# Kernel optimization log

Measured on AMD Instinct MI355X. Metric: run time of the kernel, lower is better.

Reference implementation:

```python
import jax, jax.numpy as jnp
import numpy as np

WINDOW = (2, 6, 12)  # (Wz, Wh, Ww), N = 144
HEADS = 6
TYPE_OF_WINDOWS = 10


def _position_index(ws):
    Wz, Wh, Ww = ws
    zi = np.arange(Wz); zj = -np.arange(Wz) * Wz
    hi = np.arange(Wh); hj = -np.arange(Wh) * Wh
    w = np.arange(Ww)
    c1 = np.stack(np.meshgrid(zi, hi, w, indexing='ij')).reshape(3, -1)
    c2 = np.stack(np.meshgrid(zj, hj, w, indexing='ij')).reshape(3, -1)
    coords = (c1[:, :, None] - c2[:, None, :]).transpose(1, 2, 0).copy()
    coords[:, :, 2] += Ww - 1
    coords[:, :, 1] *= 2 * Ww - 1
    coords[:, :, 0] *= (2 * Ww - 1) * Wh * Wh
    return coords.sum(-1).reshape(-1)  # [N*N]


def setup_inputs() -> dict:
    key = jax.random.key(0)
    ks = jax.random.split(key, 7)
    B, nW, C = 96, TYPE_OF_WINDOWS, 192
    N = WINDOW[0] * WINDOW[1] * WINDOW[2]
    bias_len = (2 * WINDOW[2] - 1) * WINDOW[1] ** 2 * WINDOW[0] ** 2
    return {
        'x': jax.random.normal(ks[0], (B, nW, N, C), jnp.float32),
        'mask': jax.random.normal(ks[1], (B, N, N), jnp.float32),
        'w_qkv': jax.random.normal(ks[2], (C, 3 * C), jnp.float32) * 0.02,
        'b_qkv': jnp.zeros((3 * C,), jnp.float32),
        'w_proj': jax.random.normal(ks[3], (C, C), jnp.float32) * 0.02,
        'b_proj': jnp.zeros((C,), jnp.float32),
        'bias_table': jax.random.normal(ks[4], (bias_len, nW, HEADS), jnp.float32) * 0.02,
        'position_index': jnp.asarray(_position_index(WINDOW), jnp.int32),
    }


def reference(x, mask, w_qkv, b_qkv, w_proj, b_proj, bias_table, position_index):
    B, nW, N, C = x.shape
    H = HEADS
    Dh = C // H
    scale = Dh ** -0.5
    qkv = x @ w_qkv + b_qkv                       # [B,nW,N,3C]
    qkv = qkv.reshape(B, nW, N, 3, H, Dh)
    qkv = qkv.transpose(3, 0, 1, 4, 2, 5)         # [3,B,nW,H,N,Dh]
    q, k, v = qkv[0], qkv[1], qkv[2]
    attn = jnp.einsum('bwhnd,bwhmd->bwhnm', q * scale, k)   # [B,nW,H,N,N]
    bias = bias_table[position_index]             # [N*N,nW,H]
    bias = bias.reshape(N, N, nW, H).transpose(2, 3, 0, 1)  # [nW,H,N,N]
    attn = attn + bias[None] + mask[:, None, None, :, :]
    attn = jax.nn.softmax(attn, axis=-1)
    out = jnp.einsum('bwhnm,bwhmd->bwhnd', attn, v)         # [B,nW,H,N,Dh]
    out = out.transpose(0, 1, 3, 2, 4).reshape(B, nW, N, C)
    return out @ w_proj + b_proj
```

## Files before the change

kernel.cpp:

```cpp
#include <hip/hip_runtime.h>
#include <hip/hip_bf16.h>
#include <math.h>

#define B_   96
#define NW   10
#define NN   144
#define CC   192
#define HH   6
#define DH   32
#define SCALE 0.17677669529663687f

#define XP 200
#define PP 152
#define NBW (B_ * NW)
#define QKV_STRIDE (NN * DH)

typedef __attribute__((ext_vector_type(8))) short v8s;
typedef __attribute__((ext_vector_type(4))) unsigned short v4us;
typedef __attribute__((ext_vector_type(4))) float v4f;

__device__ __forceinline__ unsigned short f2b(float f) {
  __hip_bfloat16 h = __float2bfloat16(f);
  return *reinterpret_cast<unsigned short*>(&h);
}
__device__ __forceinline__ float b2f(unsigned short s) {
  union { unsigned u; float f; } v; v.u = ((unsigned)s) << 16;
  return v.f;
}

#define N_WQT (576*192)
#define N_WPT (192*192)
#define N_BIAS (NW*HH*NN*NN)

__global__ __launch_bounds__(256) void prep_kernel(
    const float* __restrict__ w_qkv, const float* __restrict__ w_proj,
    const float* __restrict__ bias_table, const int* __restrict__ pos,
    unsigned short* __restrict__ wqT, unsigned short* __restrict__ wpT,
    unsigned short* __restrict__ biasNN)
{
  int i = blockIdx.x * 256 + threadIdx.x;
  if (i < N_WQT) {
    int n = i / 192, k = i % 192;
    wqT[i] = f2b(w_qkv[k * 576 + n]);
  } else if (i < N_WQT + N_WPT) {
    int j = i - N_WQT;
    int n = j / 192, k = j % 192;
    wpT[j] = f2b(w_proj[k * 192 + n]);
  } else if (i < N_WQT + N_WPT + N_BIAS) {
    int j = i - (N_WQT + N_WPT);
    int m = j % NN, n = (j / NN) % NN, h = (j / (NN * NN)) % HH, w = j / (NN * NN * HH);
    biasNN[j] = f2b(bias_table[(pos[n * NN + m] * NW + w) * HH + h]);
  }
}

__global__ __launch_bounds__(256, 2) void qkv_gemm(
    const float* __restrict__ x, const float* __restrict__ b_qkv,
    const unsigned short* __restrict__ wqT,
    unsigned short* __restrict__ qkv, int bw0)
{
  __shared__ unsigned short xs[NN * XP];
  const int tid  = threadIdx.x;
  const int wave = tid >> 6, lane = tid & 63;
  const int lr = lane & 15, lk8 = (lane >> 4) * 8, quad = lane >> 4;
  const int bwl = blockIdx.x;
  const int bw  = bw0 + bwl;

  const float4* xp4 = (const float4*)(x + (size_t)bw * NN * CC);
  for (int i = tid; i < NN * (CC / 4); i += 256) {
    float4 f = xp4[i];
    int r = i / (CC / 4), c = (i % (CC / 4)) * 4;
    v4us pk;
    pk[0] = f2b(f.x); pk[1] = f2b(f.y); pk[2] = f2b(f.z); pk[3] = f2b(f.w);
    *(v4us*)&xs[r * XP + c] = pk;
  }
  __syncthreads();

  v8s bf0[6], bf1[6];
  {
    const unsigned short* w0 = wqT + (size_t)(wave * 16 + lr) * CC;
    #pragma unroll
    for (int ks = 0; ks < 6; ks++) bf0[ks] = *(const v8s*)&w0[ks * 32 + lk8];
  }

  #pragma unroll
  for (int i = 0; i < 9; i++) {
    const int c = wave + i * 4;
    if (i + 1 < 9) {
      const unsigned short* wn = wqT + (size_t)((c + 4) * 16 + lr) * CC;
      if (i & 1) {
        #pragma unroll
        for (int ks = 0; ks < 6; ks++) bf0[ks] = *(const v8s*)&wn[ks * 32 + lk8];
      } else {
        #pragma unroll
        for (int ks = 0; ks < 6; ks++) bf1[ks] = *(const v8s*)&wn[ks * 32 + lk8];
      }
    }

    const int s = c / 12;
    const int h = (c % 12) >> 1;
    const int dhalf = c & 1;
    const float bv = b_qkv[c * 16 + lr];
    v4f acc[9];
    #pragma unroll
    for (int ii = 0; ii < 9; ii++) acc[ii] = (v4f){bv, bv, bv, bv};

    #pragma unroll
    for (int ks = 0; ks < 6; ks++) {
      v8s at[9];
      #pragma unroll
      for (int ii = 0; ii < 9; ii++)
        at[ii] = *(const v8s*)&xs[(ii * 16 + lr) * XP + ks * 32 + lk8];
      if (i & 1) {
        #pragma unroll
        for (int ii = 0; ii < 9; ii++)
          acc[ii] = __builtin_amdgcn_mfma_f32_16x16x32_bf16(at[ii], bf1[ks], acc[ii], 0, 0, 0);
      } else {
        #pragma unroll
        for (int ii = 0; ii < 9; ii++)
          acc[ii] = __builtin_amdgcn_mfma_f32_16x16x32_bf16(at[ii], bf0[ks], acc[ii], 0, 0, 0);
      }
    }

    if (s == 2) {
      unsigned short* opT = qkv + ((size_t)(bwl * HH + h) * 3 + 2) * QKV_STRIDE
                          + (size_t)(dhalf * 16 + lr) * NN;
      #pragma unroll
      for (int ii = 0; ii < 9; ii++) {
        const int n0 = ii * 16 + quad * 4;
        v4us pk;
        #pragma unroll
        for (int r = 0; r < 4; r++) pk[r] = f2b(acc[ii][r]);
        *(v4us*)&opT[n0] = pk;
      }
    } else {
      unsigned short* op = qkv + ((size_t)(bwl * HH + h) * 3 + s) * QKV_STRIDE + dhalf * 16 + lr;
      #pragma unroll
      for (int ii = 0; ii < 9; ii++)
        #pragma unroll
        for (int r = 0; r < 4; r++) {
          const int n = ii * 16 + quad * 4 + r;
          op[n * DH] = f2b(acc[ii][r]);
        }
    }
  }
}

__global__ __launch_bounds__(256, 3) void attn_bwh(
    const unsigned short* __restrict__ qkv, const float* __restrict__ mask,
    const unsigned short* __restrict__ biasNN,
    unsigned short* __restrict__ ao, int bw0)
{
  __shared__ unsigned short Ps[NN * PP];

  const int tid  = threadIdx.x;
  const int wave = tid >> 6, lane = tid & 63;
  const int lr = lane & 15, lk8 = (lane >> 4) * 8, quad = lane >> 4;

  const int bwl = blockIdx.x / HH;
  const int h   = blockIdx.x % HH;
  const int bw  = bw0 + bwl;
  const int b   = bw / NW;
  const int w   = bw % NW;

  const unsigned short* qp = qkv + (size_t)(bwl * HH + h) * 3 * QKV_STRIDE;
  const unsigned short* kp = qp + QKV_STRIDE;
  const unsigned short* vT = qp + 2 * QKV_STRIDE;

  v8s bv[2][4], bvt[2];
  #pragma unroll
  for (int dh2 = 0; dh2 < 2; dh2++) {
    const unsigned short* vrow = vT + (size_t)(dh2 * 16 + lr) * NN;
    #pragma unroll
    for (int ks = 0; ks < 4; ks++) bv[dh2][ks] = *(const v8s*)&vrow[ks * 32 + lk8];
    bvt[dh2] = *(const v8s*)&vrow[128 + (lk8 & 8)];
  }

  v8s aq[9];
  #pragma unroll
  for (int nt = 0; nt < 9; nt++)
    aq[nt] = *(const v8s*)&qp[(nt * 16 + lr) * DH + lk8];

  for (int mt = wave; mt < 9; mt += 4) {
    v8s bk = *(const v8s*)&kp[(mt * 16 + lr) * DH + lk8];
    const int m = mt * 16 + lr;
    #pragma unroll
    for (int nt = 0; nt < 9; nt++) {
      v4f c = {0.f, 0.f, 0.f, 0.f};
      c = __builtin_amdgcn_mfma_f32_16x16x32_bf16(aq[nt], bk, c, 0, 0, 0);
      #pragma unroll
      for (int r = 0; r < 4; r++) {
        const int n = nt * 16 + quad * 4 + r;
        Ps[n * PP + m] = f2b(c[r] * SCALE);
      }
    }
  }
  __syncthreads();

  const unsigned short* bp = biasNN + (size_t)(w * HH + h) * NN * NN;
  const float* mp = mask + (size_t)b * NN * NN;
  for (int rr = 0; rr < 9; rr++) {
    const int row = rr * 16 + wave * 4 + quad;
    unsigned short* prow = &Ps[row * PP];
    const unsigned short* brow = bp + (size_t)row * NN;
    const float* mrow = mp + (size_t)row * NN;
    float bm[9];
    #pragma unroll
    for (int j = 0; j < 9; j++)
      bm[j] = b2f(brow[j * 16 + lr]) + mrow[j * 16 + lr];
    float e[9];
    float mx = -1e30f;
    #pragma unroll
    for (int j = 0; j < 9; j++) {
      e[j] = b2f(prow[j * 16 + lr]) + bm[j];
      mx = fmaxf(mx, e[j]);
    }
    #pragma unroll
    for (int off = 8; off; off >>= 1) mx = fmaxf(mx, __shfl_xor(mx, off, 64));
    float s = 0.f;
    #pragma unroll
    for (int j = 0; j < 9; j++) { e[j] = __expf(e[j] - mx); s += e[j]; }
    #pragma unroll
    for (int off = 8; off; off >>= 1) s += __shfl_xor(s, off, 64);
    const float inv = 1.f / s;
    #pragma unroll
    for (int j = 0; j < 9; j++) prow[j * 16 + lr] = f2b(e[j] * inv);
  }
  __syncthreads();

  const v8s vzero = {};
  for (int nt = wave; nt < 9; nt += 4) {
    v8s ap[4];
    #pragma unroll
    for (int ks = 0; ks < 4; ks++)
      ap[ks] = *(const v8s*)&Ps[(nt * 16 + lr) * PP + ks * 32 + lk8];
    v8s at = *(const v8s*)&Ps[(nt * 16 + lr) * PP + 128 + (lk8 & 8)];
    at = (quad < 2) ? at : vzero;
    #pragma unroll
    for (int dh2 = 0; dh2 < 2; dh2++) {
      v4f c = {0.f, 0.f, 0.f, 0.f};
      #pragma unroll
      for (int ks = 0; ks < 4; ks++)
        c = __builtin_amdgcn_mfma_f32_16x16x32_bf16(ap[ks], bv[dh2][ks], c, 0, 0, 0);
      c = __builtin_amdgcn_mfma_f32_16x16x32_bf16(at, bvt[dh2], c, 0, 0, 0);
      #pragma unroll
      for (int r = 0; r < 4; r++) {
        const int n = nt * 16 + quad * 4 + r;
        ao[((size_t)bw * NN + n) * CC + h * DH + dh2 * 16 + lr] = f2b(c[r]);
      }
    }
  }
}

__global__ __launch_bounds__(256) void proj_mfma(
    const unsigned short* __restrict__ ao,
    const unsigned short* __restrict__ wpT,
    const float* __restrict__ b_proj,
    float* __restrict__ out)
{
  const int tid  = threadIdx.x;
  const int wave = tid >> 6, lane = tid & 63;
  const int lr = lane & 15, lk8 = (lane >> 4) * 8, quad = lane >> 4;
  const size_t row0 = (size_t)blockIdx.x * 64;
  const int j0 = wave * 3;

  v8s bf[3][6];
  #pragma unroll
  for (int jj = 0; jj < 3; jj++)
    #pragma unroll
    for (int ks = 0; ks < 6; ks++)
      bf[jj][ks] = *(const v8s*)(wpT + (size_t)((j0 + jj) * 16 + lr) * CC + ks * 32 + lk8);

  float bvj[3];
  #pragma unroll
  for (int jj = 0; jj < 3; jj++) bvj[jj] = b_proj[(j0 + jj) * 16 + lr];

  #pragma unroll
  for (int rt = 0; rt < 4; rt++) {
    const size_t r0 = row0 + rt * 16;
    v8s a[6];
    #pragma unroll
    for (int ks = 0; ks < 6; ks++)
      a[ks] = *(const v8s*)(ao + (r0 + lr) * CC + ks * 32 + lk8);
    v4f acc[3];
    #pragma unroll
    for (int jj = 0; jj < 3; jj++) acc[jj] = (v4f){bvj[jj], bvj[jj], bvj[jj], bvj[jj]};
    #pragma unroll
    for (int ks = 0; ks < 6; ks++)
      #pragma unroll
      for (int jj = 0; jj < 3; jj++)
        acc[jj] = __builtin_amdgcn_mfma_f32_16x16x32_bf16(a[ks], bf[jj][ks], acc[jj], 0, 0, 0);
    #pragma unroll
    for (int jj = 0; jj < 3; jj++)
      #pragma unroll
      for (int r = 0; r < 4; r++)
        out[(r0 + quad * 4 + r) * CC + (j0 + jj) * 16 + lr] = acc[jj][r];
  }
}

extern "C" void kernel_launch(void* const* d_in, const int* in_sizes, int n_in,
                              void* d_out, int out_size, void* d_ws, size_t ws_size,
                              hipStream_t stream)
{
  const float* x          = (const float*)d_in[0];
  const float* mask       = (const float*)d_in[1];
  const float* w_qkv      = (const float*)d_in[2];
  const float* b_qkv      = (const float*)d_in[3];
  const float* w_proj     = (const float*)d_in[4];
  const float* b_proj     = (const float*)d_in[5];
  const float* bias_table = (const float*)d_in[6];
  const int*   pos        = (const int*)d_in[7];
  float* out = (float*)d_out;

  unsigned short* biasNN = (unsigned short*)d_ws;
  unsigned short* wqT    = biasNN + N_BIAS;
  unsigned short* wpT    = wqT + N_WQT;
  unsigned short* ao     = wpT + N_WPT;
  unsigned short* qkvws  = ao + (size_t)B_ * NW * NN * CC;

  const size_t fixed_bytes = (size_t)(qkvws - (unsigned short*)d_ws) * sizeof(unsigned short);
  const size_t per_bw      = (size_t)HH * 3 * QKV_STRIDE * sizeof(unsigned short);
  size_t avail = (ws_size > fixed_bytes) ? (ws_size - fixed_bytes) : 0;
  int maxchunk = (int)(avail / per_bw);
  if (maxchunk < 60)  maxchunk = 60;
  if (maxchunk > NBW) maxchunk = NBW;
  const int npass = (NBW + maxchunk - 1) / maxchunk;
  const int chunk = (NBW + npass - 1) / npass;

  const int prep_total = N_WQT + N_WPT + N_BIAS;
  prep_kernel<<<(prep_total + 255) / 256, 256, 0, stream>>>(
      w_qkv, w_proj, bias_table, pos, wqT, wpT, biasNN);

  for (int bw0 = 0; bw0 < NBW; bw0 += chunk) {
    const int cur = (NBW - bw0 < chunk) ? (NBW - bw0) : chunk;
    qkv_gemm<<<cur, 256, 0, stream>>>(x, b_qkv, wqT, qkvws, bw0);
    attn_bwh<<<cur * HH, 256, 0, stream>>>(qkvws, mask, biasNN, ao, bw0);
  }
  proj_mfma<<<(B_ * NW * NN) / 64, 256, 0, stream>>>(ao, wpT, b_proj, out);
}
```

Before: 439.6 us.

## Fuse QK^T, softmax and PV per query tile in registers, shrink LDS

```diff
diff --git a/kernel.cpp b/kernel.cpp
--- a/kernel.cpp
+++ b/kernel.cpp
@@ -150,7 +150,7 @@
     const unsigned short* __restrict__ biasNN,
     unsigned short* __restrict__ ao, int bw0)
 {
-  __shared__ unsigned short Ps[NN * PP];
+  __shared__ unsigned short Ps[4 * 16 * PP];
 
   const int tid  = threadIdx.x;
   const int wave = tid >> 6, lane = tid & 63;
@@ -175,65 +175,64 @@
     bvt[dh2] = *(const v8s*)&vrow[128 + (lk8 & 8)];
   }
 
-  v8s aq[9];
-  #pragma unroll
-  for (int nt = 0; nt < 9; nt++)
-    aq[nt] = *(const v8s*)&qp[(nt * 16 + lr) * DH + lk8];
-
-  for (int mt = wave; mt < 9; mt += 4) {
-    v8s bk = *(const v8s*)&kp[(mt * 16 + lr) * DH + lk8];
-    const int m = mt * 16 + lr;
-    #pragma unroll
-    for (int nt = 0; nt < 9; nt++) {
-      v4f c = {0.f, 0.f, 0.f, 0.f};
-      c = __builtin_amdgcn_mfma_f32_16x16x32_bf16(aq[nt], bk, c, 0, 0, 0);
-      #pragma unroll
-      for (int r = 0; r < 4; r++) {
-        const int n = nt * 16 + quad * 4 + r;
-        Ps[n * PP + m] = f2b(c[r] * SCALE);
-      }
-    }
-  }
-  __syncthreads();
-
   const unsigned short* bp = biasNN + (size_t)(w * HH + h) * NN * NN;
   const float* mp = mask + (size_t)b * NN * NN;
-  for (int rr = 0; rr < 9; rr++) {
-    const int row = rr * 16 + wave * 4 + quad;
-    unsigned short* prow = &Ps[row * PP];
-    const unsigned short* brow = bp + (size_t)row * NN;
-    const float* mrow = mp + (size_t)row * NN;
-    float bm[9];
-    #pragma unroll
-    for (int j = 0; j < 9; j++)
-      bm[j] = b2f(brow[j * 16 + lr]) + mrow[j * 16 + lr];
-    float e[9];
-    float mx = -1e30f;
-    #pragma unroll
-    for (int j = 0; j < 9; j++) {
-      e[j] = b2f(prow[j * 16 + lr]) + bm[j];
-      mx = fmaxf(mx, e[j]);
-    }
-    #pragma unroll
-    for (int off = 8; off; off >>= 1) mx = fmaxf(mx, __shfl_xor(mx, off, 64));
-    float s = 0.f;
-    #pragma unroll
-    for (int j = 0; j < 9; j++) { e[j] = __expf(e[j] - mx); s += e[j]; }
-    #pragma unroll
-    for (int off = 8; off; off >>= 1) s += __shfl_xor(s, off, 64);
-    const float inv = 1.f / s;
-    #pragma unroll
-    for (int j = 0; j < 9; j++) prow[j * 16 + lr] = f2b(e[j] * inv);
-  }
-  __syncthreads();
-
+  unsigned short* Pw = &Ps[wave * 16 * PP];
   const v8s vzero = {};
-  for (int nt = wave; nt < 9; nt += 4) {
+
+  auto process_nt = [&](int nt) {
+    v8s aq = *(const v8s*)&qp[(nt * 16 + lr) * DH + lk8];
+    v4f acc[9];
+    #pragma unroll
+    for (int mt = 0; mt < 9; mt++) {
+      v8s bk = *(const v8s*)&kp[(mt * 16 + lr) * DH + lk8];
+      v4f z = {0.f, 0.f, 0.f, 0.f};
+      acc[mt] = __builtin_amdgcn_mfma_f32_16x16x32_bf16(aq, bk, z, 0, 0, 0);
+    }
+    float mx[4] = {-1e30f, -1e30f, -1e30f, -1e30f};
+    #pragma unroll
+    for (int r = 0; r < 4; r++) {
+      const int row = nt * 16 + quad * 4 + r;
+      const unsigned short* br = bp + (size_t)row * NN;
+      const float* mr = mp + (size_t)row * NN;
+      #pragma unroll
+      for (int mt = 0; mt < 9; mt++) {
+        float v = fmaf(acc[mt][r], SCALE, b2f(br[mt * 16 + lr]) + mr[mt * 16 + lr]);
+        acc[mt][r] = v;
+        mx[r] = fmaxf(mx[r], v);
+      }
+    }
+    #pragma unroll
+    for (int r = 0; r < 4; r++)
+      #pragma unroll
+      for (int off = 8; off; off >>= 1)
+        mx[r] = fmaxf(mx[r], __shfl_xor(mx[r], off, 64));
+    float sum[4] = {0.f, 0.f, 0.f, 0.f};
+    #pragma unroll
+    for (int r = 0; r < 4; r++)
+      #pragma unroll
+      for (int mt = 0; mt < 9; mt++) {
+        float e = __expf(acc[mt][r] - mx[r]);
+        acc[mt][r] = e;
+        sum[r] += e;
+      }
+    #pragma unroll
+    for (int r = 0; r < 4; r++)
+      #pragma unroll
+      for (int off = 8; off; off >>= 1)
+        sum[r] += __shfl_xor(sum[r], off, 64);
+    #pragma unroll
+    for (int r = 0; r < 4; r++) {
+      const float inv = 1.f / sum[r];
+      #pragma unroll
+      for (int mt = 0; mt < 9; mt++)
+        Pw[(quad * 4 + r) * PP + mt * 16 + lr] = f2b(acc[mt][r] * inv);
+    }
     v8s ap[4];
     #pragma unroll
     for (int ks = 0; ks < 4; ks++)
-      ap[ks] = *(const v8s*)&Ps[(nt * 16 + lr) * PP + ks * 32 + lk8];
-    v8s at = *(const v8s*)&Ps[(nt * 16 + lr) * PP + 128 + (lk8 & 8)];
+      ap[ks] = *(const v8s*)&Pw[lr * PP + ks * 32 + lk8];
+    v8s at = *(const v8s*)&Pw[lr * PP + 128 + (lk8 & 8)];
     at = (quad < 2) ? at : vzero;
     #pragma unroll
     for (int dh2 = 0; dh2 < 2; dh2++) {
@@ -248,7 +247,11 @@
         ao[((size_t)bw * NN + n) * CC + h * DH + dh2 * 16 + lr] = f2b(c[r]);
       }
     }
-  }
+  };
+
+  process_nt(wave);
+  process_nt(wave + 4);
+  if (wave == 0) process_nt(8);
 }
 
 __global__ __launch_bounds__(256) void proj_mfma(
```

Measured after the change: 473.1 us. 1.08x slower.
